# Kernel optimization log

Hardware: AMD Instinct MI355X
Metric: run time of the kernel (lower is better)

## Reference

```python
import jax, jax.numpy as jnp
import numpy as np

B, D1, DJ, S, OUT = 8, 1024, 512, 2048, 2048
IN = D1 + 2 * DJ  # linear input_dim = 2048


def setup_inputs() -> dict:
    key = jax.random.key(0)
    k1, k2, k3, kw, kb = jax.random.split(key, 5)
    return {
        "input1": jax.random.normal(k1, (B, D1, S), dtype=jnp.float32),
        "input2_a": jax.random.normal(k2, (B, DJ, S), dtype=jnp.float32),
        "input2_b": jax.random.normal(k3, (B, DJ, S), dtype=jnp.float32),
        "W": jax.random.normal(kw, (OUT, IN), dtype=jnp.float32) * (1.0 / np.sqrt(IN)),
        "b": jax.random.normal(kb, (OUT,), dtype=jnp.float32) * 0.01,
    }


def reference(input1, input2_a, input2_b, W, b):
    # Original loops over seq_len, per-step concat along feature dim then linear.
    # Fused: concat along feature axis once, transpose to [B, S, F], one GEMM.
    x = jnp.concatenate([input1, input2_a, input2_b], axis=1)  # [B, IN, S]
    x = jnp.transpose(x, (0, 2, 1))                            # [B, S, IN]
    out = jnp.einsum('bsf,of->bso', x, W) + b                  # [B, S, OUT]
    return out
```

## Files before the change

kernel.cpp:

```cpp
#include <hip/hip_runtime.h>
#include <hip/hip_bf16.h>

#define B_   8
#define D1_  1024
#define DJ_  512
#define S_   2048
#define OUT_ 2048
#define IN_  2048
#define M_TOT (B_ * S_)

typedef __attribute__((ext_vector_type(8))) short          bf16x8;
typedef __attribute__((ext_vector_type(8))) unsigned short ushort8;
typedef __attribute__((ext_vector_type(4))) float          f32x4;

typedef __attribute__((address_space(3))) unsigned int as3_uint;
typedef __attribute__((address_space(1))) unsigned int as1_uint;

__device__ __forceinline__ unsigned short f2bf(float f) {
    union { float f; unsigned u; } v; v.f = f;
    unsigned r = v.u + 0x7FFF + ((v.u >> 16) & 1);
    return (unsigned short)(r >> 16);
}

__device__ __forceinline__ void gload_lds16(const void* g, const void* l) {
    __builtin_amdgcn_global_load_lds(
        (const as1_uint*)(unsigned long long)g,
        (as3_uint*)(unsigned int)(unsigned long long)l,
        16, 0, 0);
}

__global__ __launch_bounds__(256) void transpose_convert_kernel(
        const float* __restrict__ in1, const float* __restrict__ in2a,
        const float* __restrict__ in2b, unsigned short* __restrict__ Xt) {
    __shared__ float tile[64][65];
    int bid = blockIdx.x;
    int st = bid & 31;
    int ft = (bid >> 5) & 31;
    int b  = bid >> 10;
    int f0 = ft << 6, s0 = st << 6;

    const float* src; int frel;
    if (f0 < D1_)             { src = in1  + (size_t)b * D1_ * S_; frel = f0; }
    else if (f0 < D1_ + DJ_)  { src = in2a + (size_t)b * DJ_ * S_; frel = f0 - D1_; }
    else                      { src = in2b + (size_t)b * DJ_ * S_; frel = f0 - (D1_ + DJ_); }

    int t = threadIdx.x;
    int tr = t >> 4, tc = t & 15;
    #pragma unroll
    for (int i = 0; i < 4; ++i) {
        int fi = tr + i * 16;
        const float4 v = *reinterpret_cast<const float4*>(
            &src[(size_t)(frel + fi) * S_ + s0 + tc * 4]);
        tile[fi][tc * 4 + 0] = v.x; tile[fi][tc * 4 + 1] = v.y;
        tile[fi][tc * 4 + 2] = v.z; tile[fi][tc * 4 + 3] = v.w;
    }
    __syncthreads();
    int si0 = t >> 3, fx = t & 7;
    #pragma unroll
    for (int i = 0; i < 2; ++i) {
        int si = si0 + i * 32;
        ushort8 h;
        #pragma unroll
        for (int j = 0; j < 8; ++j) h[j] = f2bf(tile[fx * 8 + j][si]);
        *reinterpret_cast<ushort8*>(
            &Xt[(size_t)(b * S_ + s0 + si) * IN_ + f0 + fx * 8]) = h;
    }
}

__global__ __launch_bounds__(256) void convert_w_kernel(
        const float* __restrict__ W, unsigned short* __restrict__ Wb) {
    size_t i = (size_t)blockIdx.x * 256 + threadIdx.x;
    const float4* p = reinterpret_cast<const float4*>(W) + i * 2;
    float4 a = p[0], c = p[1];
    ushort8 h;
    h[0] = f2bf(a.x); h[1] = f2bf(a.y); h[2] = f2bf(a.z); h[3] = f2bf(a.w);
    h[4] = f2bf(c.x); h[5] = f2bf(c.y); h[6] = f2bf(c.z); h[7] = f2bf(c.w);
    *(reinterpret_cast<ushort8*>(Wb) + i) = h;
}


__global__ __launch_bounds__(512, 2) void gemm256_kernel(
        const unsigned short* __restrict__ A,
        const unsigned short* __restrict__ Bm,
        const float* __restrict__ bias,
        float* __restrict__ C) {
    __shared__ unsigned short As_[32768];
    __shared__ unsigned short Bs_[32768];

    int bid = blockIdx.x;
    int swz = (bid & 7) * 64 + (bid >> 3);
    int m0 = (swz >> 3) * 256;
    int n0 = (swz & 7) * 256;

    int t = threadIdx.x;
    int lane = t & 63, wave = t >> 6;
    int wm = wave >> 2;
    int wn = wave & 3;
    int fr = lane & 15;
    int fkslot = lane >> 4;

    int sr  = t >> 3;
    int sc  = t & 7;
    int swc = sc ^ (sr & 7);

    int sl0 = ((fkslot)     ^ (fr & 7)) * 8;
    int sl1 = ((4 + fkslot) ^ (fr & 7)) * 8;
    int arow = wm * 64 + fr;
    int brow = wn * 32 + fr;

#define STAGE_A(bb, h, kt) do { \
    const unsigned short* _g0 = A + (size_t)(m0 + (h)*64 + sr) * IN_ + (kt) + swc*8; \
    const unsigned short* _g1 = A + (size_t)(m0 + 128 + (h)*64 + sr) * IN_ + (kt) + swc*8; \
    unsigned short* _l = As_ + ((bb)*2 + (h))*8192 + sr*64 + sc*8; \
    gload_lds16(_g0, _l); \
    gload_lds16(_g1, _l + 4096); \
} while (0)

#define STAGE_B(bb, h, kt) do { \
    const unsigned short* _g0 = Bm + (size_t)(n0 + (sr>>5)*64 + (h)*32 + (sr&31)) * IN_ + (kt) + swc*8; \
    const unsigned short* _g1 = Bm + (size_t)(n0 + 128 + (sr>>5)*64 + (h)*32 + (sr&31)) * IN_ + (kt) + swc*8; \
    unsigned short* _l = Bs_ + ((bb)*2 + (h))*8192 + sr*64 + sc*8; \
    gload_lds16(_g0, _l); \
    gload_lds16(_g1, _l + 4096); \
} while (0)

#define READ_A(bb, qm) do { \
    const unsigned short* _Ab = As_ + ((bb)*2 + (qm))*8192; \
    _Pragma("unroll") \
    for (int i = 0; i < 4; ++i) { \
        int rr = (arow + i*16) * 64; \
        a_[i][0] = *reinterpret_cast<const bf16x8*>(_Ab + rr + sl0); \
        a_[i][1] = *reinterpret_cast<const bf16x8*>(_Ab + rr + sl1); \
    } \
} while (0)

#define READ_B(bb, qn) do { \
    const unsigned short* _Bb = Bs_ + ((bb)*2 + (qn))*8192; \
    _Pragma("unroll") \
    for (int j = 0; j < 2; ++j) { \
        int rr = (brow + j*16) * 64; \
        b_[j][0] = *reinterpret_cast<const bf16x8*>(_Bb + rr + sl0); \
        b_[j][1] = *reinterpret_cast<const bf16x8*>(_Bb + rr + sl1); \
    } \
} while (0)

#define VMW asm volatile("s_waitcnt vmcnt(4)" ::: "memory")

#define PHASE(qm, qn, READ_STMT, STAGE_STMT, VM_STMT) do { \
    READ_STMT; \
    STAGE_STMT; \
    __builtin_amdgcn_s_barrier(); \
    asm volatile("s_waitcnt lgkmcnt(0)" ::: "memory"); \
    __builtin_amdgcn_sched_barrier(0); \
    __builtin_amdgcn_s_setprio(1); \
    _Pragma("unroll") \
    for (int i = 0; i < 4; ++i) { \
        _Pragma("unroll") \
        for (int j = 0; j < 2; ++j) { \
            acc[(qm)*4+i][(qn)*2+j] = __builtin_amdgcn_mfma_f32_16x16x32_bf16( \
                a_[i][0], b_[j][0], acc[(qm)*4+i][(qn)*2+j], 0, 0, 0); \
            acc[(qm)*4+i][(qn)*2+j] = __builtin_amdgcn_mfma_f32_16x16x32_bf16( \
                a_[i][1], b_[j][1], acc[(qm)*4+i][(qn)*2+j], 0, 0, 0); \
        } \
    } \
    __builtin_amdgcn_s_setprio(0); \
    VM_STMT; \
    __builtin_amdgcn_s_barrier(); \
} while (0)

    f32x4 acc[8][4] = {};
    bf16x8 a_[4][2], b_[2][2];

    STAGE_A(0, 0, 0);  STAGE_A(0, 1, 0);
    STAGE_B(0, 0, 0);  STAGE_B(0, 1, 0);
    STAGE_A(1, 0, 64); STAGE_B(1, 1, 64);
    asm volatile("s_waitcnt vmcnt(4)" ::: "memory");
    __builtin_amdgcn_s_barrier();

    for (int it = 0; it < IN_ / 128; ++it) {
        int k1 = it * 128 + 64;
        int k2 = (it * 128 + 128) & (IN_ - 1);
        int k3 = (it * 128 + 192) & (IN_ - 1);
        PHASE(0, 0, { READ_A(0, 0); READ_B(0, 0); }, STAGE_A(1, 1, k1), );
        PHASE(0, 1, READ_B(0, 1),                    STAGE_B(1, 0, k1), );
        PHASE(1, 1, READ_A(0, 1),                    STAGE_A(0, 0, k2), );
        PHASE(1, 0, READ_B(0, 0),                    STAGE_B(0, 1, k2), VMW);
        PHASE(0, 0, { READ_A(1, 0); READ_B(1, 0); }, STAGE_A(0, 1, k2), );
        PHASE(0, 1, READ_B(1, 1),                    STAGE_B(0, 0, k2), );
        PHASE(1, 1, READ_A(1, 1),                    STAGE_A(1, 0, k3), );
        PHASE(1, 0, READ_B(1, 0),                    STAGE_B(1, 1, k3), VMW);
    }

    float bv[4];
    #pragma unroll
    for (int n_ = 0; n_ < 4; ++n_) bv[n_] = bias[n0 + wn * 64 + n_ * 16 + fr];
    int crow0 = m0 + wm * 128 + (lane >> 4) * 4;
    int ccol0 = n0 + wn * 64 + fr;
    #pragma unroll
    for (int mi = 0; mi < 8; ++mi) {
        #pragma unroll
        for (int r_ = 0; r_ < 4; ++r_) {
            float* cp = C + (size_t)(crow0 + mi * 16 + r_) * OUT_ + ccol0;
            #pragma unroll
            for (int n_ = 0; n_ < 4; ++n_) cp[n_ * 16] = acc[mi][n_][r_] + bv[n_];
        }
    }
#undef STAGE_A
#undef STAGE_B
#undef READ_A
#undef READ_B
#undef VMW
#undef PHASE
}

__global__ __launch_bounds__(256) void naive_kernel(
        const float* __restrict__ in1, const float* __restrict__ in2a,
        const float* __restrict__ in2b, const float* __restrict__ W,
        const float* __restrict__ bias, float* __restrict__ out) {
    size_t id = (size_t)blockIdx.x * 256 + threadIdx.x;
    int s = (int)(id & (S_ - 1));
    size_t bo = id >> 11;
    int o = (int)(bo & (OUT_ - 1));
    int b = (int)(bo >> 11);
    const float* w = W + (size_t)o * IN_;
    float acc = bias[o];
    const float* x1 = in1 + (size_t)b * D1_ * S_ + s;
    for (int f = 0; f < D1_; ++f) acc += x1[(size_t)f * S_] * w[f];
    const float* x2 = in2a + (size_t)b * DJ_ * S_ + s;
    for (int f = 0; f < DJ_; ++f) acc += x2[(size_t)f * S_] * w[D1_ + f];
    const float* x3 = in2b + (size_t)b * DJ_ * S_ + s;
    for (int f = 0; f < DJ_; ++f) acc += x3[(size_t)f * S_] * w[D1_ + DJ_ + f];
    out[((size_t)b * S_ + s) * OUT_ + o] = acc;
}

extern "C" void kernel_launch(void* const* d_in, const int* in_sizes, int n_in,
                              void* d_out, int out_size, void* d_ws, size_t ws_size,
                              hipStream_t stream) {
    const float* in1  = (const float*)d_in[0];
    const float* in2a = (const float*)d_in[1];
    const float* in2b = (const float*)d_in[2];
    const float* W    = (const float*)d_in[3];
    const float* bias = (const float*)d_in[4];
    float* out = (float*)d_out;

    const size_t xt_bytes = (size_t)M_TOT * IN_ * 2;
    const size_t wb_bytes = (size_t)OUT_ * IN_ * 2;

    if (ws_size < xt_bytes + wb_bytes) {
        naive_kernel<<<(B_ * (size_t)OUT_ * S_) / 256, 256, 0, stream>>>(
            in1, in2a, in2b, W, bias, out);
        return;
    }

    unsigned short* Xt = (unsigned short*)d_ws;
    unsigned short* Wb = (unsigned short*)((char*)d_ws + xt_bytes);

    transpose_convert_kernel<<<B_ * 32 * 32, 256, 0, stream>>>(in1, in2a, in2b, Xt);
    convert_w_kernel<<<(OUT_ * IN_) / (256 * 8), 256, 0, stream>>>(W, Wb);
    gemm256_kernel<<<(M_TOT / 256) * (OUT_ / 256), 512, 0, stream>>>(Xt, Wb, bias, out);
}
```

Baseline: 169.5 us.

## Double-buffer MFMA fragment registers to prefetch LDS reads one phase ahead

Splits the A/B fragment registers into several named buffers so each phase's LDS reads fetch operands for the next phase while the current phase's MFMAs consume already-loaded registers. The full lgkmcnt(0) waits become partial waits, and the global-load wait is moved and tightened to vmcnt(2), reordering when staged tiles are consumed. The aim is to hide LDS read latency behind matrix math, at the cost of extra VGPRs and a more fragile hand-tuned wait/ordering scheme that could race if the counts are wrong.

```diff
diff --git a/kernel.cpp b/kernel.cpp
--- a/kernel.cpp
+++ b/kernel.cpp
@@ -124,33 +124,34 @@
     gload_lds16(_g1, _l + 4096); \
 } while (0)
 
-#define READ_A(bb, qm) do { \
+#define READ_A(bb, qm, DST) do { \
     const unsigned short* _Ab = As_ + ((bb)*2 + (qm))*8192; \
     _Pragma("unroll") \
     for (int i = 0; i < 4; ++i) { \
         int rr = (arow + i*16) * 64; \
-        a_[i][0] = *reinterpret_cast<const bf16x8*>(_Ab + rr + sl0); \
-        a_[i][1] = *reinterpret_cast<const bf16x8*>(_Ab + rr + sl1); \
+        DST[i][0] = *reinterpret_cast<const bf16x8*>(_Ab + rr + sl0); \
+        DST[i][1] = *reinterpret_cast<const bf16x8*>(_Ab + rr + sl1); \
     } \
 } while (0)
 
-#define READ_B(bb, qn) do { \
+#define READ_B(bb, qn, DST) do { \
     const unsigned short* _Bb = Bs_ + ((bb)*2 + (qn))*8192; \
     _Pragma("unroll") \
     for (int j = 0; j < 2; ++j) { \
         int rr = (brow + j*16) * 64; \
-        b_[j][0] = *reinterpret_cast<const bf16x8*>(_Bb + rr + sl0); \
-        b_[j][1] = *reinterpret_cast<const bf16x8*>(_Bb + rr + sl1); \
+        DST[j][0] = *reinterpret_cast<const bf16x8*>(_Bb + rr + sl0); \
+        DST[j][1] = *reinterpret_cast<const bf16x8*>(_Bb + rr + sl1); \
     } \
 } while (0)
 
-#define VMW asm volatile("s_waitcnt vmcnt(4)" ::: "memory")
-
-#define PHASE(qm, qn, READ_STMT, STAGE_STMT, VM_STMT) do { \
+#define VMW asm volatile("s_waitcnt vmcnt(2)" ::: "memory")
+
+#define PHASE(qm, qn, AR, BR, READ_STMT, STAGE_STMT, LGN, VM_STMT) do { \
     READ_STMT; \
+    __builtin_amdgcn_sched_barrier(0); \
     STAGE_STMT; \
     __builtin_amdgcn_s_barrier(); \
-    asm volatile("s_waitcnt lgkmcnt(0)" ::: "memory"); \
+    asm volatile("s_waitcnt lgkmcnt(" #LGN ")" ::: "memory"); \
     __builtin_amdgcn_sched_barrier(0); \
     __builtin_amdgcn_s_setprio(1); \
     _Pragma("unroll") \
@@ -158,9 +159,9 @@
         _Pragma("unroll") \
         for (int j = 0; j < 2; ++j) { \
             acc[(qm)*4+i][(qn)*2+j] = __builtin_amdgcn_mfma_f32_16x16x32_bf16( \
-                a_[i][0], b_[j][0], acc[(qm)*4+i][(qn)*2+j], 0, 0, 0); \
+                AR[i][0], BR[j][0], acc[(qm)*4+i][(qn)*2+j], 0, 0, 0); \
             acc[(qm)*4+i][(qn)*2+j] = __builtin_amdgcn_mfma_f32_16x16x32_bf16( \
-                a_[i][1], b_[j][1], acc[(qm)*4+i][(qn)*2+j], 0, 0, 0); \
+                AR[i][1], BR[j][1], acc[(qm)*4+i][(qn)*2+j], 0, 0, 0); \
         } \
     } \
     __builtin_amdgcn_s_setprio(0); \
@@ -169,26 +170,29 @@
 } while (0)
 
     f32x4 acc[8][4] = {};
-    bf16x8 a_[4][2], b_[2][2];
+    bf16x8 aX[4][2], aY[4][2];
+    bf16x8 bC[2][2], bD[2][2], bE[2][2];
 
     STAGE_A(0, 0, 0);  STAGE_A(0, 1, 0);
     STAGE_B(0, 0, 0);  STAGE_B(0, 1, 0);
     STAGE_A(1, 0, 64); STAGE_B(1, 1, 64);
     asm volatile("s_waitcnt vmcnt(4)" ::: "memory");
     __builtin_amdgcn_s_barrier();
+    READ_A(0, 0, aX);
+    READ_B(0, 0, bC);
 
     for (int it = 0; it < IN_ / 128; ++it) {
         int k1 = it * 128 + 64;
         int k2 = (it * 128 + 128) & (IN_ - 1);
         int k3 = (it * 128 + 192) & (IN_ - 1);
-        PHASE(0, 0, { READ_A(0, 0); READ_B(0, 0); }, STAGE_A(1, 1, k1), );
-        PHASE(0, 1, READ_B(0, 1),                    STAGE_B(1, 0, k1), );
-        PHASE(1, 1, READ_A(0, 1),                    STAGE_A(0, 0, k2), );
-        PHASE(1, 0, READ_B(0, 0),                    STAGE_B(0, 1, k2), VMW);
-        PHASE(0, 0, { READ_A(1, 0); READ_B(1, 0); }, STAGE_A(0, 1, k2), );
-        PHASE(0, 1, READ_B(1, 1),                    STAGE_B(0, 0, k2), );
-        PHASE(1, 1, READ_A(1, 1),                    STAGE_A(1, 0, k3), );
-        PHASE(1, 0, READ_B(1, 0),                    STAGE_B(1, 1, k3), VMW);
+        PHASE(0, 0, aX, bC, READ_B(0, 1, bD),                        STAGE_A(1, 1, k1), 4,  );
+        PHASE(0, 1, aX, bD, READ_A(0, 1, aY),                        STAGE_B(1, 0, k1), 8,  );
+        PHASE(1, 1, aY, bD, ,                                        STAGE_A(0, 0, k2), 0,  VMW);
+        PHASE(1, 0, aY, bC, { READ_A(1, 0, aX); READ_B(1, 0, bE); }, STAGE_B(0, 1, k2), 12, );
+        PHASE(0, 0, aX, bE, READ_B(1, 1, bD),                        STAGE_A(0, 1, k2), 4,  );
+        PHASE(0, 1, aX, bD, READ_A(1, 1, aY),                        STAGE_B(0, 0, k2), 8,  );
+        PHASE(1, 1, aY, bD, ,                                        STAGE_A(1, 0, k3), 0,  VMW);
+        PHASE(1, 0, aY, bE, { READ_A(0, 0, aX); READ_B(0, 0, bC); }, STAGE_B(1, 1, k3), 12, );
     }
 
     float bv[4];
```

After: 174.4 us. +2.9%, slower.

## Merge prep kernels and halve GEMM barriers per k-step

Applied to the files above, without the earlier changes.

The transpose/convert kernel and the W conversion kernel become one launch, with the W blocks appended after the transpose blocks, which saves a kernel launch and the gap between launches. The GEMM main loop goes from eight barrier-delimited phases per iteration to four super-phases. Each super-phase runs two MFMA groups separated only by an LDS wait, dropping the barrier that came before each MFMA block. This removes about half of the workgroup barriers, but the LDS buffer reuse hazards now rest on the reordered staging and wait placement.

```diff
diff --git a/kernel.cpp b/kernel.cpp
--- a/kernel.cpp
+++ b/kernel.cpp
@@ -29,11 +29,22 @@
         16, 0, 0);
 }
 
-__global__ __launch_bounds__(256) void transpose_convert_kernel(
+__global__ __launch_bounds__(256) void prep_kernel(
         const float* __restrict__ in1, const float* __restrict__ in2a,
-        const float* __restrict__ in2b, unsigned short* __restrict__ Xt) {
+        const float* __restrict__ in2b, const float* __restrict__ W,
+        unsigned short* __restrict__ Xt, unsigned short* __restrict__ Wb) {
+    int bid = blockIdx.x;
+    if (bid >= 8192) {
+        size_t i = (size_t)(bid - 8192) * 256 + threadIdx.x;
+        const float4* p = reinterpret_cast<const float4*>(W) + i * 2;
+        float4 a = p[0], c = p[1];
+        ushort8 h;
+        h[0] = f2bf(a.x); h[1] = f2bf(a.y); h[2] = f2bf(a.z); h[3] = f2bf(a.w);
+        h[4] = f2bf(c.x); h[5] = f2bf(c.y); h[6] = f2bf(c.z); h[7] = f2bf(c.w);
+        *(reinterpret_cast<ushort8*>(Wb) + i) = h;
+        return;
+    }
     __shared__ float tile[64][65];
-    int bid = blockIdx.x;
     int st = bid & 31;
     int ft = (bid >> 5) & 31;
     int b  = bid >> 10;
@@ -65,17 +76,6 @@
         *reinterpret_cast<ushort8*>(
             &Xt[(size_t)(b * S_ + s0 + si) * IN_ + f0 + fx * 8]) = h;
     }
-}
-
-__global__ __launch_bounds__(256) void convert_w_kernel(
-        const float* __restrict__ W, unsigned short* __restrict__ Wb) {
-    size_t i = (size_t)blockIdx.x * 256 + threadIdx.x;
-    const float4* p = reinterpret_cast<const float4*>(W) + i * 2;
-    float4 a = p[0], c = p[1];
-    ushort8 h;
-    h[0] = f2bf(a.x); h[1] = f2bf(a.y); h[2] = f2bf(a.z); h[3] = f2bf(a.w);
-    h[4] = f2bf(c.x); h[5] = f2bf(c.y); h[6] = f2bf(c.z); h[7] = f2bf(c.w);
-    *(reinterpret_cast<ushort8*>(Wb) + i) = h;
 }
 
 
@@ -144,15 +144,7 @@
     } \
 } while (0)
 
-#define VMW asm volatile("s_waitcnt vmcnt(4)" ::: "memory")
-
-#define PHASE(qm, qn, READ_STMT, STAGE_STMT, VM_STMT) do { \
-    READ_STMT; \
-    STAGE_STMT; \
-    __builtin_amdgcn_s_barrier(); \
-    asm volatile("s_waitcnt lgkmcnt(0)" ::: "memory"); \
-    __builtin_amdgcn_sched_barrier(0); \
-    __builtin_amdgcn_s_setprio(1); \
+#define MFMA4(qm, qn) \
     _Pragma("unroll") \
     for (int i = 0; i < 4; ++i) { \
         _Pragma("unroll") \
@@ -162,7 +154,43 @@
             acc[(qm)*4+i][(qn)*2+j] = __builtin_amdgcn_mfma_f32_16x16x32_bf16( \
                 a_[i][1], b_[j][1], acc[(qm)*4+i][(qn)*2+j], 0, 0, 0); \
         } \
-    } \
+    }
+
+#define LGKM0 do { \
+    asm volatile("s_waitcnt lgkmcnt(0)" ::: "memory"); \
+    __builtin_amdgcn_sched_barrier(0); \
+} while (0)
+
+#define VMW asm volatile("s_waitcnt vmcnt(4)" ::: "memory")
+
+#define SP_EVEN(bb, S1, S2, VM_STMT) do { \
+    READ_B(bb, 0); \
+    READ_A(bb, 0); \
+    S1; S2; \
+    LGKM0; \
+    __builtin_amdgcn_s_setprio(1); \
+    MFMA4(0, 0) \
+    __builtin_amdgcn_s_setprio(0); \
+    READ_B(bb, 1); \
+    LGKM0; \
+    __builtin_amdgcn_s_setprio(1); \
+    MFMA4(0, 1) \
+    __builtin_amdgcn_s_setprio(0); \
+    VM_STMT; \
+    __builtin_amdgcn_s_barrier(); \
+} while (0)
+
+#define SP_ODD(bb, S1, S2, VM_STMT) do { \
+    READ_A(bb, 1); \
+    S1; S2; \
+    LGKM0; \
+    __builtin_amdgcn_s_setprio(1); \
+    MFMA4(1, 1) \
+    __builtin_amdgcn_s_setprio(0); \
+    READ_B(bb, 0); \
+    LGKM0; \
+    __builtin_amdgcn_s_setprio(1); \
+    MFMA4(1, 0) \
     __builtin_amdgcn_s_setprio(0); \
     VM_STMT; \
     __builtin_amdgcn_s_barrier(); \
@@ -181,14 +209,10 @@
         int k1 = it * 128 + 64;
         int k2 = (it * 128 + 128) & (IN_ - 1);
         int k3 = (it * 128 + 192) & (IN_ - 1);
-        PHASE(0, 0, { READ_A(0, 0); READ_B(0, 0); }, STAGE_A(1, 1, k1), );
-        PHASE(0, 1, READ_B(0, 1),                    STAGE_B(1, 0, k1), );
-        PHASE(1, 1, READ_A(0, 1),                    STAGE_A(0, 0, k2), );
-        PHASE(1, 0, READ_B(0, 0),                    STAGE_B(0, 1, k2), VMW);
-        PHASE(0, 0, { READ_A(1, 0); READ_B(1, 0); }, STAGE_A(0, 1, k2), );
-        PHASE(0, 1, READ_B(1, 1),                    STAGE_B(0, 0, k2), );
-        PHASE(1, 1, READ_A(1, 1),                    STAGE_A(1, 0, k3), );
-        PHASE(1, 0, READ_B(1, 0),                    STAGE_B(1, 1, k3), VMW);
+        SP_EVEN(0, STAGE_A(1, 1, k1), STAGE_B(1, 0, k1), );
+        SP_ODD (0, STAGE_A(0, 0, k2), STAGE_B(0, 1, k2), VMW);
+        SP_EVEN(1, STAGE_A(0, 1, k2), STAGE_B(0, 0, k2), );
+        SP_ODD (1, STAGE_A(1, 0, k3), STAGE_B(1, 1, k3), VMW);
     }
 
     float bv[4];
@@ -209,8 +233,11 @@
 #undef STAGE_B
 #undef READ_A
 #undef READ_B
+#undef MFMA4
+#undef LGKM0
 #undef VMW
-#undef PHASE
+#undef SP_EVEN
+#undef SP_ODD
 }
 
 __global__ __launch_bounds__(256) void naive_kernel(
@@ -255,7 +282,7 @@
     unsigned short* Xt = (unsigned short*)d_ws;
     unsigned short* Wb = (unsigned short*)((char*)d_ws + xt_bytes);
 
-    transpose_convert_kernel<<<B_ * 32 * 32, 256, 0, stream>>>(in1, in2a, in2b, Xt);
-    convert_w_kernel<<<(OUT_ * IN_) / (256 * 8), 256, 0, stream>>>(W, Wb);
+    prep_kernel<<<8192 + (OUT_ * IN_) / (256 * 8), 256, 0, stream>>>(
+        in1, in2a, in2b, W, Xt, Wb);
     gemm256_kernel<<<(M_TOT / 256) * (OUT_ / 256), 512, 0, stream>>>(Xt, Wb, bias, out);
 }
```

After: 162.7 us. 4.0% less time.
